# Kernel tuning notes

Measured on AMD Instinct MI355X. Metric: run time of the kernel, lower is better.

Reference implementation:

```python
import jax, jax.numpy as jnp
import numpy as np

B, L, D, H, DH = 2, 2048, 1024, 16, 64
THETA_T = 100.0
EPS_COS = 1e-6
EPS_NORM = 1e-6


def make_rope_tables(n_heads=H, d_head=DH, theta_t=THETA_T):
    dr = d_head // 12                      # 5 rotary freqs per head per axis
    n = n_heads * dr
    log_min, log_max = np.log(np.pi), np.log(10.0 * np.pi)
    f = np.exp(np.linspace(log_min, log_max, n + 1)[:-1])
    freqs = np.stack([f, f]).reshape(2, dr, n_heads).transpose(0, 2, 1)   # (2, H, dr)
    t_freqs = (theta_t ** (-np.arange(n, dtype=np.float64) / n)).reshape(dr, n_heads).T  # (H, dr)
    return jnp.asarray(freqs, jnp.float32), jnp.asarray(t_freqs, jnp.float32)


def rms_norm(x, scale, eps=EPS_NORM):
    ms = jnp.mean(x.astype(jnp.float32) ** 2, axis=-1, keepdims=True)
    return x * (scale.astype(jnp.float32) * jax.lax.rsqrt(ms + eps)).astype(x.dtype)


def rope_theta(pos, pos_orig, time, freqs, t_freqs):
    # pos_to_use: (b, l, c=2, xy=2), mapped to [-1, 1]
    pos_use = jnp.stack([pos_orig, pos], axis=2) * 2.0 - 1.0
    theta_w = pos_use[..., 0][:, :, :, None, None] * freqs[0]      # b l 2 H dr
    theta_h = pos_use[..., 1][:, :, :, None, None] * freqs[1]      # b l 2 H dr
    theta_t = time[:, :, None, None, None] * t_freqs               # b l 1 H dr
    theta = jnp.concatenate([theta_h, theta_w, theta_t], axis=2)   # b l 5 H dr
    b, l = theta.shape[0], theta.shape[1]
    theta = jnp.transpose(theta, (0, 1, 3, 2, 4)).reshape(b, l, H, -1)  # b l H (5*dr)
    return theta


def apply_rotary_emb(x, theta):
    d = theta.shape[-1]
    x1, x2, x3 = x[..., :d], x[..., d:2 * d], x[..., 2 * d:]
    cos, sin = jnp.cos(theta), jnp.sin(theta)
    y1 = x1 * cos - x2 * sin
    y2 = x2 * cos + x1 * sin
    return jnp.concatenate([y1, y2, x3], axis=-1)


def scale_for_cosine_sim(q, k, scale, eps=EPS_COS):
    sq = jnp.sum(q * q, axis=-1, keepdims=True)
    sk = jnp.sum(k * k, axis=-1, keepdims=True)
    sqrt_scale = jnp.sqrt(scale)                         # (H,1,1) -> broadcasts to (b,H,l,1)
    return q * (sqrt_scale * jax.lax.rsqrt(sq + eps)), k * (sqrt_scale * jax.lax.rsqrt(sk + eps))


def setup_inputs() -> dict:
    key = jax.random.key(0)
    ks = jax.random.split(key, 8)
    return {
        "x": jax.random.normal(ks[0], (B, L, D), jnp.float32),
        "pos": jax.random.uniform(ks[1], (B, L, 2), jnp.float32),
        "pos_orig": jax.random.uniform(ks[2], (B, L, 2), jnp.float32),
        "time": jax.random.uniform(ks[3], (B, L), jnp.float32),
        "w_qkv": jax.random.normal(ks[4], (3 * D, D), jnp.float32) * (D ** -0.5),
        "w_out": jax.random.normal(ks[5], (D, D), jnp.float32) * (D ** -0.5),
        "w_up": jax.random.normal(ks[6], (4 * D, D), jnp.float32) * (D ** -0.5),
        "w_down": jax.random.normal(ks[7], (D, 4 * D), jnp.float32) * ((4 * D) ** -0.5),
        "norm1_scale": jnp.ones((D,), jnp.float32),
        "norm2_scale": jnp.ones((D,), jnp.float32),
        "qk_scale": jnp.full((H, 1, 1), 10.0, jnp.float32),
    }


def reference(x, pos, pos_orig, time, w_qkv, w_out, w_up, w_down,
              norm1_scale, norm2_scale, qk_scale):
    freqs, t_freqs = make_rope_tables()
    b, l, _ = x.shape

    # --- attention block (pre-norm) ---
    xn = rms_norm(x, norm1_scale)
    qkv = jnp.einsum('bld,ed->ble', xn, w_qkv)                  # b l 3D
    q, k, v = jnp.split(qkv, 3, axis=-1)
    q = q.reshape(b, l, H, DH)
    k = k.reshape(b, l, H, DH)
    v = v.reshape(b, l, H, DH).transpose(0, 2, 1, 3)            # b H l dh

    theta = rope_theta(pos, pos_orig, time, freqs, t_freqs)      # b l H 25
    q = apply_rotary_emb(q, theta).transpose(0, 2, 1, 3)         # b H l dh
    k = apply_rotary_emb(k, theta).transpose(0, 2, 1, 3)

    q, k = scale_for_cosine_sim(q, k, qk_scale)                  # cosine-sim QK norm
    scores = jnp.einsum('bhqd,bhkd->bhqk', q, k)                 # scale=1 (already folded in)
    probs = jax.nn.softmax(scores, axis=-1)
    attn = jnp.einsum('bhqk,bhkd->bhqd', probs, v)
    attn = attn.transpose(0, 2, 1, 3).reshape(b, l, D)
    x = x + jnp.einsum('bld,ed->ble', attn, w_out)

    h = rms_norm(x, norm2_scale)
    h = jax.nn.gelu(jnp.einsum('bld,ed->ble', h, w_up), approximate=True)
    x = x + jnp.einsum('ble,de->bld', h, w_down)
    return x
```

## Files before the change

### kernel.cpp

```cpp
#include <hip/hip_runtime.h>

#define B_ 2
#define L_ 2048
#define D_ 1024
#define H_ 16
#define DH_ 64

typedef float f32x4 __attribute__((ext_vector_type(4)));
typedef __bf16 bf16x8 __attribute__((ext_vector_type(8)));

__device__ __forceinline__ ushort f2bf(float f) {
  unsigned u = __float_as_uint(f);
  u += 0x7fffu + ((u >> 16) & 1u);
  return (ushort)(u >> 16);
}
__device__ __forceinline__ float bf2f(ushort h) {
  return __uint_as_float(((unsigned)h) << 16);
}

__device__ __forceinline__ void gload_lds16(const void* g, void* l) {
  __builtin_amdgcn_global_load_lds(
      (const __attribute__((address_space(1))) unsigned*)g,
      (__attribute__((address_space(3))) unsigned*)l, 16, 0, 0);
}

__global__ __launch_bounds__(256) void cast_bf16_kernel(const float* __restrict__ in,
                                                        ushort* __restrict__ out, int n4) {
  int i = blockIdx.x * 256 + threadIdx.x;
  if (i >= n4) return;
  float4 v = ((const float4*)in)[i];
  ushort4 o;
  o.x = f2bf(v.x); o.y = f2bf(v.y); o.z = f2bf(v.z); o.w = f2bf(v.w);
  ((ushort4*)out)[i] = o;
}

__global__ __launch_bounds__(256) void rmsnorm_kernel(const float* __restrict__ x,
                                                      const float* __restrict__ scale,
                                                      ushort* __restrict__ out) {
  int row = blockIdx.x, t = threadIdx.x;
  float4 v = ((const float4*)(x + (size_t)row * D_))[t];
  float ss = v.x * v.x + v.y * v.y + v.z * v.z + v.w * v.w;
#pragma unroll
  for (int d = 1; d < 64; d <<= 1) ss += __shfl_xor(ss, d);
  __shared__ float wsum[4];
  if ((t & 63) == 0) wsum[t >> 6] = ss;
  __syncthreads();
  float tot = wsum[0] + wsum[1] + wsum[2] + wsum[3];
  float r = rsqrtf(tot * (1.0f / D_) + 1e-6f);
  float4 sc = ((const float4*)scale)[t];
  ushort4 o;
  o.x = f2bf(v.x * sc.x * r); o.y = f2bf(v.y * sc.y * r);
  o.z = f2bf(v.z * sc.z * r); o.w = f2bf(v.w * sc.w * r);
  ((ushort4*)(out + (size_t)row * D_))[t] = o;
}

template <int EPI, int BM, int BN, int DEPTH, int XR>
__global__ __launch_bounds__(256) void gemm_nt(const ushort* __restrict__ A,
                                               const ushort* __restrict__ Bw,
                                               void* __restrict__ Cout,
                                               const float* __restrict__ resid,
                                               int M, int N, int K) {
  constexpr int WROWS = BM / 2, WCOLS = BN / 2;
  constexpr int MR = WROWS / 16, NR = WCOLS / 16;
  constexpr int ALOADS = BM / 64, BLOADS = BN / 64;
  constexpr int NLOADS = ALOADS + BLOADS;
  constexpr int XC = 8 / XR;
  __shared__ __align__(16) ushort Als[DEPTH][BM * 32];
  __shared__ __align__(16) ushort Bls[DEPTH][BN * 32];
  const int tid = threadIdx.x;
  const int lane = tid & 63;
  const int w = tid >> 6;
  const int wr = w >> 1, wc = w & 1;
  const int bid = blockIdx.y * gridDim.x + blockIdx.x;
  const int xcd = bid & 7;
  const int i = bid >> 3;
  const int CR = gridDim.x / XR, CC = gridDim.y / XC;
  const int rt = (xcd % XR) * CR + (i % CR);
  const int ct = (xcd / XR) * CC + (i / CR);
  const int row0 = rt * BM;
  const int col0 = ct * BN;
  const ushort* Ab = A + (size_t)row0 * K;
  const ushort* Bb = Bw + (size_t)col0 * K;
  const int sr = tid >> 2;
  const int scA = (((tid & 3) ^ ((tid >> 3) & 3)) * 8);
  const int fr = lane & 15;
  const int fg = lane >> 4;
  f32x4 zero = {0.f, 0.f, 0.f, 0.f};
  f32x4 acc[MR][NR];
#pragma unroll
  for (int m = 0; m < MR; m++)
#pragma unroll
    for (int n = 0; n < NR; n++) acc[m][n] = zero;

  auto stage = [&](int buf, int kt) {
#pragma unroll
    for (int i2 = 0; i2 < ALOADS; i2++)
      gload_lds16(Ab + (size_t)(sr + 64 * i2) * K + kt + scA, &Als[buf][i2 * 2048 + tid * 8]);
#pragma unroll
    for (int i2 = 0; i2 < BLOADS; i2++)
      gload_lds16(Bb + (size_t)(sr + 64 * i2) * K + kt + scA, &Bls[buf][i2 * 2048 + tid * 8]);
  };
  const int nt = K >> 5;
#pragma unroll
  for (int p = 0; p < DEPTH - 1; p++) stage(p, p << 5);
  int cur = 0, sbuf = DEPTH - 1;
  for (int t = 0; t < nt; t++) {
    const int ahead = nt - 1 - t;
    if constexpr (DEPTH == 3) {
      if (ahead >= 1) asm volatile("s_waitcnt vmcnt(%0)" ::"i"(NLOADS) : "memory");
      else            asm volatile("s_waitcnt vmcnt(0)" ::: "memory");
    } else {
      if (ahead >= 3)      asm volatile("s_waitcnt vmcnt(%0)" ::"i"(3 * NLOADS) : "memory");
      else if (ahead == 2) asm volatile("s_waitcnt vmcnt(%0)" ::"i"(2 * NLOADS) : "memory");
      else if (ahead == 1) asm volatile("s_waitcnt vmcnt(%0)" ::"i"(NLOADS) : "memory");
      else                 asm volatile("s_waitcnt vmcnt(0)" ::: "memory");
    }
    __builtin_amdgcn_s_barrier();
    __builtin_amdgcn_sched_barrier(0);
    if (t + DEPTH - 1 < nt) {
      stage(sbuf, (t + DEPTH - 1) << 5);
      sbuf = (sbuf == DEPTH - 1) ? 0 : sbuf + 1;
    }
    bf16x8 af[MR], bfr[NR];
#pragma unroll
    for (int m = 0; m < MR; m++) {
      int rA = wr * WROWS + m * 16 + fr;
      af[m] = *(const bf16x8*)&Als[cur][rA * 32 + ((fg ^ ((rA >> 1) & 3)) << 3)];
    }
#pragma unroll
    for (int n = 0; n < NR; n++) {
      int rB = wc * WCOLS + n * 16 + fr;
      bfr[n] = *(const bf16x8*)&Bls[cur][rB * 32 + ((fg ^ ((rB >> 1) & 3)) << 3)];
    }
    __builtin_amdgcn_s_setprio(1);
#pragma unroll
    for (int m = 0; m < MR; m++)
#pragma unroll
      for (int n = 0; n < NR; n++)
        acc[m][n] = __builtin_amdgcn_mfma_f32_16x16x32_bf16(af[m], bfr[n], acc[m][n], 0, 0, 0);
    __builtin_amdgcn_s_setprio(0);
    cur = (cur == DEPTH - 1) ? 0 : cur + 1;
  }
  const int orow = row0 + wr * WROWS + fg * 4;
  const int ocol = col0 + wc * WCOLS + fr;
#pragma unroll
  for (int m = 0; m < MR; m++) {
#pragma unroll
    for (int j = 0; j < 4; j++) {
      int r = orow + m * 16 + j;
#pragma unroll
      for (int n = 0; n < NR; n++) {
        int cidx = ocol + n * 16;
        size_t idx = (size_t)r * N + cidx;
        float v = acc[m][n][j];
        if (EPI == 0) {
          ((ushort*)Cout)[idx] = f2bf(v);
        } else if (EPI == 1) {
          ((float*)Cout)[idx] = resid[idx] + v;
        } else {
          float g = 0.5f * v * (1.0f + tanhf(0.7978845608f * (v + 0.044715f * v * v * v)));
          ((ushort*)Cout)[idx] = f2bf(g);
        }
      }
    }
  }
}

__global__ __launch_bounds__(256) void rope_kernel(const ushort* __restrict__ qkv,
                                                   const float* __restrict__ pos,
                                                   const float* __restrict__ pos_orig,
                                                   const float* __restrict__ timep,
                                                   const float* __restrict__ qk_scale,
                                                   ushort* __restrict__ qr,
                                                   ushort* __restrict__ kr) {
  int gw = (blockIdx.x * 256 + threadIdx.x) >> 6;
  int lane = threadIdx.x & 63;
  int h = gw & 15;
  int row = gw >> 4;
  int b = row >> 11;
  int l = row & (L_ - 1);
  float qv = bf2f(qkv[(size_t)row * 3072 + h * 64 + lane]);
  float kv = bf2f(qkv[(size_t)row * 3072 + 1024 + h * 64 + lane]);
  float c = 1.0f, s = 0.0f;
  if (lane < 50) {
    int idx = lane < 25 ? lane : lane - 25;
    int sg = idx / 5, d = idx % 5;
    int fi = d * 16 + h;
    float th;
    if (sg == 4) {
      th = timep[row] * __expf(-(float)fi * 0.05756462732485115f);
    } else {
      float fr = 3.14159265358979323846f * __expf((float)fi * 0.028782313662425575f);
      const float* psrc = (sg == 0 || sg == 2) ? pos_orig : pos;
      int comp = (sg < 2) ? 1 : 0;
      th = (2.0f * psrc[(size_t)row * 2 + comp] - 1.0f) * fr;
    }
    s = sinf(th);
    c = cosf(th);
  }
  int partner = lane < 25 ? lane + 25 : lane - 25;
  float qp = __shfl(qv, partner, 64);
  float kp = __shfl(kv, partner, 64);
  float yq, yk;
  if (lane < 25) { yq = qv * c - qp * s; yk = kv * c - kp * s; }
  else if (lane < 50) { yq = qv * c + qp * s; yk = kv * c + kp * s; }
  else { yq = qv; yk = kv; }
  float sq = yq * yq, sk = yk * yk;
#pragma unroll
  for (int d = 1; d < 64; d <<= 1) { sq += __shfl_xor(sq, d); sk += __shfl_xor(sk, d); }
  float scl = sqrtf(qk_scale[h]);
  float qo = yq * scl * rsqrtf(sq + 1e-6f);
  float ko = yk * scl * rsqrtf(sk + 1e-6f);
  size_t o = ((size_t)(b * 16 + h) * L_ + l) * 64 + lane;
  qr[o] = f2bf(qo);
  kr[o] = f2bf(ko);
}

__global__ __launch_bounds__(256) void vtrans_kernel(const ushort* __restrict__ qkv,
                                                     ushort* __restrict__ vT) {
  __shared__ __align__(16) ushort tile[64][72];
  int t = threadIdx.x;
  int lt = blockIdx.x;
  int bh = blockIdx.y;
  int b = bh >> 4, h = bh & 15;
  int r = t >> 3, c0 = (t & 7) * 8;
#pragma unroll
  for (int half = 0; half < 2; half++) {
    const ushort* src =
        qkv + (size_t)(b * L_ + lt * 64 + r + half * 32) * 3072 + 2048 + h * 64 + c0;
    *(uint4*)&tile[r + half * 32][c0] = *(const uint4*)src;
  }
  __syncthreads();
#pragma unroll
  for (int half = 0; half < 2; half++) {
    int dh = r + half * 32;
    unsigned p0 = (unsigned)tile[c0 + 0][dh] | ((unsigned)tile[c0 + 1][dh] << 16);
    unsigned p1 = (unsigned)tile[c0 + 2][dh] | ((unsigned)tile[c0 + 3][dh] << 16);
    unsigned p2 = (unsigned)tile[c0 + 4][dh] | ((unsigned)tile[c0 + 5][dh] << 16);
    unsigned p3 = (unsigned)tile[c0 + 6][dh] | ((unsigned)tile[c0 + 7][dh] << 16);
    uint4 o; o.x = p0; o.y = p1; o.z = p2; o.w = p3;
    *(uint4*)&vT[((size_t)bh * 64 + dh) * L_ + lt * 64 + c0] = o;
  }
}

__global__ __launch_bounds__(256) void attn_kernel(const ushort* __restrict__ qr,
                                                   const ushort* __restrict__ kr,
                                                   const ushort* __restrict__ vT,
                                                   ushort* __restrict__ attnb) {
  __shared__ __align__(16) ushort Kls[2][64 * 64];
  __shared__ __align__(16) ushort Vls[2][64 * 64];
  __shared__ __align__(16) ushort Pls[4][16 * 64];
  const int tid = threadIdx.x, lane = tid & 63, w = tid >> 6;
  const int qt = blockIdx.x, bh = blockIdx.y;
  const int b = bh >> 4;
  const int fr = lane & 15, fg = lane >> 4;
  const ushort* Qb = qr + ((size_t)bh * L_ + qt * 64 + w * 16) * 64;
  bf16x8 qf[2];
#pragma unroll
  for (int c = 0; c < 2; c++)
    qf[c] = *(const bf16x8*)(Qb + fr * 64 + c * 32 + fg * 8);
  f32x4 zero = {0.f, 0.f, 0.f, 0.f};
  f32x4 accO[4];
#pragma unroll
  for (int n = 0; n < 4; n++) accO[n] = zero;
  float lrow[4] = {0.f, 0.f, 0.f, 0.f};
  const int sr = tid >> 3;
  const int scz = (((tid & 7) ^ (sr & 7)) * 8);
  auto stage = [&](int buf, int kt) {
    gload_lds16(kr + ((size_t)bh * L_ + kt + sr) * 64 + scz, &Kls[buf][tid * 8]);
    gload_lds16(kr + ((size_t)bh * L_ + kt + 32 + sr) * 64 + scz, &Kls[buf][2048 + tid * 8]);
    gload_lds16(vT + ((size_t)bh * 64 + sr) * L_ + kt + scz, &Vls[buf][tid * 8]);
    gload_lds16(vT + ((size_t)bh * 64 + 32 + sr) * L_ + kt + scz, &Vls[buf][2048 + tid * 8]);
  };
  stage(0, 0);
  int cur = 0;
  for (int t = 0; t < (L_ >> 6); t++) {
    asm volatile("s_waitcnt vmcnt(0)" ::: "memory");
    __builtin_amdgcn_s_barrier();
    __builtin_amdgcn_sched_barrier(0);
    if (t + 1 < (L_ >> 6)) stage(cur ^ 1, (t + 1) << 6);
    f32x4 sv[4];
#pragma unroll
    for (int n = 0; n < 4; n++) sv[n] = zero;
    __builtin_amdgcn_s_setprio(1);
#pragma unroll
    for (int c = 0; c < 2; c++) {
#pragma unroll
      for (int n = 0; n < 4; n++) {
        bf16x8 kf =
            *(const bf16x8*)&Kls[cur][(n * 16 + fr) * 64 + (((c * 4 + fg) ^ (fr & 7)) << 3)];
        sv[n] = __builtin_amdgcn_mfma_f32_16x16x32_bf16(qf[c], kf, sv[n], 0, 0, 0);
      }
    }
    __builtin_amdgcn_s_setprio(0);
#pragma unroll
    for (int n = 0; n < 4; n++)
#pragma unroll
      for (int j = 0; j < 4; j++) {
        float p = __expf(sv[n][j] - 12.0f);
        sv[n][j] = p;
        lrow[j] += p;
      }
#pragma unroll
    for (int j = 0; j < 4; j++) {
      int row = fg * 4 + j;
      int rbase = row * 64;
      int rx = row & 7;
#pragma unroll
      for (int n = 0; n < 4; n++) {
        int chunk = 2 * n + (fr >> 3);
        Pls[w][rbase + ((chunk ^ rx) << 3) + (fr & 7)] =
            (ushort)(__float_as_uint(sv[n][j]) >> 16);
      }
    }
    __builtin_amdgcn_s_setprio(1);
#pragma unroll
    for (int c = 0; c < 2; c++) {
      bf16x8 pa = *(const bf16x8*)&Pls[w][fr * 64 + (((c * 4 + fg) ^ (fr & 7)) << 3)];
#pragma unroll
      for (int n = 0; n < 4; n++) {
        bf16x8 vb =
            *(const bf16x8*)&Vls[cur][(n * 16 + fr) * 64 + (((c * 4 + fg) ^ (fr & 7)) << 3)];
        accO[n] = __builtin_amdgcn_mfma_f32_16x16x32_bf16(pa, vb, accO[n], 0, 0, 0);
      }
    }
    __builtin_amdgcn_s_setprio(0);
    cur ^= 1;
  }
#pragma unroll
  for (int j = 0; j < 4; j++) {
#pragma unroll
    for (int d = 1; d < 16; d <<= 1) lrow[j] += __shfl_xor(lrow[j], d);
    lrow[j] = 1.0f / lrow[j];
  }
#pragma unroll
  for (int n = 0; n < 4; n++) {
#pragma unroll
    for (int j = 0; j < 4; j++) {
      float o = accO[n][j] * lrow[j];
      int qrow = qt * 64 + w * 16 + fg * 4 + j;
      int dh = fr + n * 16;
      attnb[(size_t)(b * L_ + qrow) * 1024 + (bh & 15) * 64 + dh] = f2bf(o);
    }
  }
}

extern "C" void kernel_launch(void* const* d_in, const int* in_sizes, int n_in,
                              void* d_out, int out_size, void* d_ws, size_t ws_size,
                              hipStream_t stream) {
  const float* x = (const float*)d_in[0];
  const float* pos = (const float*)d_in[1];
  const float* pos_orig = (const float*)d_in[2];
  const float* timep = (const float*)d_in[3];
  const float* w_qkv = (const float*)d_in[4];
  const float* w_out = (const float*)d_in[5];
  const float* w_up = (const float*)d_in[6];
  const float* w_down = (const float*)d_in[7];
  const float* norm1 = (const float*)d_in[8];
  const float* norm2 = (const float*)d_in[9];
  const float* qk_scale = (const float*)d_in[10];
  float* out = (float*)d_out;
  char* ws = (char*)d_ws;
  size_t off = 0;
  auto alloc = [&](size_t bytes) {
    void* p = ws + off;
    off += bytes;
    return p;
  };
  ushort* xn = (ushort*)alloc(8ull << 20);
  ushort* qkvb = (ushort*)alloc(32ull << 20);
  ushort* qrb = (ushort*)alloc(8ull << 20);
  ushort* krb = (ushort*)alloc(8ull << 20);
  ushort* vTb = (ushort*)alloc(8ull << 20);
  ushort* attnb = (ushort*)alloc(8ull << 20);
  float* x1 = (float*)alloc(16ull << 20);
  ushort* wqkvb = (ushort*)alloc(6ull << 20);
  ushort* woutb = (ushort*)alloc(2ull << 20);
  ushort* wupb = (ushort*)alloc(8ull << 20);
  ushort* wdownb = (ushort*)alloc(8ull << 20);

  cast_bf16_kernel<<<3072, 256, 0, stream>>>(w_qkv, wqkvb, 3145728 / 4);
  cast_bf16_kernel<<<1024, 256, 0, stream>>>(w_out, woutb, 1048576 / 4);
  cast_bf16_kernel<<<4096, 256, 0, stream>>>(w_up, wupb, 4194304 / 4);
  cast_bf16_kernel<<<4096, 256, 0, stream>>>(w_down, wdownb, 4194304 / 4);

  rmsnorm_kernel<<<4096, 256, 0, stream>>>(x, norm1, xn);
  gemm_nt<0, 128, 128, 3, 4><<<dim3(32, 24), 256, 0, stream>>>(xn, wqkvb, qkvb, nullptr, 4096, 3072, 1024);
  rope_kernel<<<16384, 256, 0, stream>>>(qkvb, pos, pos_orig, timep, qk_scale, qrb, krb);
  vtrans_kernel<<<dim3(32, 32), 256, 0, stream>>>(qkvb, vTb);
  attn_kernel<<<dim3(32, 32), 256, 0, stream>>>(qrb, krb, vTb, attnb);
  gemm_nt<1, 64, 64, 5, 8><<<dim3(64, 16), 256, 0, stream>>>(attnb, woutb, x1, x, 4096, 1024, 1024);
  rmsnorm_kernel<<<4096, 256, 0, stream>>>(x1, norm2, xn);
  gemm_nt<2, 128, 128, 3, 4><<<dim3(32, 32), 256, 0, stream>>>(xn, wupb, qkvb, nullptr, 4096, 4096, 1024);
  gemm_nt<1, 64, 64, 5, 8><<<dim3(64, 16), 256, 0, stream>>>(qkvb, wdownb, out, x1, 4096, 1024, 4096);
}
```

Before: 299.4 us.

## Process two K-tiles per barrier in small GEMMs and remap attention blocks to XCDs

The GEMM main loop becomes a generalized pipeline in which each barrier iteration consumes SUB K-tiles and issues SUB prefetches. The 64x64 GEMMs (out-proj and down-proj) move from depth 5 with one tile per barrier to depth 6 with two tiles per barrier, halving the number of barriers and waitcnt points. The attention kernel also remaps its block index so that consecutive blocks on the same XCD share a batch-head, which should improve K/V reuse in that XCD's L2. In exchange, each wait covers fewer tiles in flight and the deeper ring uses more LDS.

```diff
diff --git a/kernel.cpp b/kernel.cpp
--- a/kernel.cpp
+++ b/kernel.cpp
@@ -54,7 +54,7 @@
   ((ushort4*)(out + (size_t)row * D_))[t] = o;
 }
 
-template <int EPI, int BM, int BN, int DEPTH, int XR>
+template <int EPI, int BM, int BN, int DEPTH, int SUB, int XR>
 __global__ __launch_bounds__(256) void gemm_nt(const ushort* __restrict__ A,
                                                const ushort* __restrict__ Bw,
                                                void* __restrict__ Cout,
@@ -64,6 +64,8 @@
   constexpr int MR = WROWS / 16, NR = WCOLS / 16;
   constexpr int ALOADS = BM / 64, BLOADS = BN / 64;
   constexpr int NLOADS = ALOADS + BLOADS;
+  constexpr int P = DEPTH - SUB;
+  constexpr int STEADY = NLOADS * (P - SUB);
   constexpr int XC = 8 / XR;
   __shared__ __align__(16) ushort Als[DEPTH][BM * 32];
   __shared__ __align__(16) ushort Bls[DEPTH][BN * 32];
@@ -73,10 +75,10 @@
   const int wr = w >> 1, wc = w & 1;
   const int bid = blockIdx.y * gridDim.x + blockIdx.x;
   const int xcd = bid & 7;
-  const int i = bid >> 3;
+  const int i0 = bid >> 3;
   const int CR = gridDim.x / XR, CC = gridDim.y / XC;
-  const int rt = (xcd % XR) * CR + (i % CR);
-  const int ct = (xcd / XR) * CC + (i / CR);
+  const int rt = (xcd % XR) * CR + (i0 % CR);
+  const int ct = (xcd / XR) * CC + (i0 / CR);
   const int row0 = rt * BM;
   const int col0 = ct * BN;
   const ushort* Ab = A + (size_t)row0 * K;
@@ -92,54 +94,50 @@
 #pragma unroll
     for (int n = 0; n < NR; n++) acc[m][n] = zero;
 
-  auto stage = [&](int buf, int kt) {
+  auto stage = [&](int slot, int kt) {
 #pragma unroll
     for (int i2 = 0; i2 < ALOADS; i2++)
-      gload_lds16(Ab + (size_t)(sr + 64 * i2) * K + kt + scA, &Als[buf][i2 * 2048 + tid * 8]);
+      gload_lds16(Ab + (size_t)(sr + 64 * i2) * K + kt + scA, &Als[slot][i2 * 2048 + tid * 8]);
 #pragma unroll
     for (int i2 = 0; i2 < BLOADS; i2++)
-      gload_lds16(Bb + (size_t)(sr + 64 * i2) * K + kt + scA, &Bls[buf][i2 * 2048 + tid * 8]);
+      gload_lds16(Bb + (size_t)(sr + 64 * i2) * K + kt + scA, &Bls[slot][i2 * 2048 + tid * 8]);
   };
   const int nt = K >> 5;
-#pragma unroll
-  for (int p = 0; p < DEPTH - 1; p++) stage(p, p << 5);
-  int cur = 0, sbuf = DEPTH - 1;
-  for (int t = 0; t < nt; t++) {
-    const int ahead = nt - 1 - t;
-    if constexpr (DEPTH == 3) {
-      if (ahead >= 1) asm volatile("s_waitcnt vmcnt(%0)" ::"i"(NLOADS) : "memory");
-      else            asm volatile("s_waitcnt vmcnt(0)" ::: "memory");
-    } else {
-      if (ahead >= 3)      asm volatile("s_waitcnt vmcnt(%0)" ::"i"(3 * NLOADS) : "memory");
-      else if (ahead == 2) asm volatile("s_waitcnt vmcnt(%0)" ::"i"(2 * NLOADS) : "memory");
-      else if (ahead == 1) asm volatile("s_waitcnt vmcnt(%0)" ::"i"(NLOADS) : "memory");
-      else                 asm volatile("s_waitcnt vmcnt(0)" ::: "memory");
-    }
+  const int ni = nt / SUB;
+#pragma unroll
+  for (int p = 0; p < P; p++) stage(p, p << 5);
+  for (int t = 0; t < ni; t++) {
+    if (t < ni - 1) asm volatile("s_waitcnt vmcnt(%0)" ::"i"(STEADY) : "memory");
+    else            asm volatile("s_waitcnt vmcnt(0)" ::: "memory");
     __builtin_amdgcn_s_barrier();
     __builtin_amdgcn_sched_barrier(0);
-    if (t + DEPTH - 1 < nt) {
-      stage(sbuf, (t + DEPTH - 1) << 5);
-      sbuf = (sbuf == DEPTH - 1) ? 0 : sbuf + 1;
-    }
-    bf16x8 af[MR], bfr[NR];
-#pragma unroll
-    for (int m = 0; m < MR; m++) {
-      int rA = wr * WROWS + m * 16 + fr;
-      af[m] = *(const bf16x8*)&Als[cur][rA * 32 + ((fg ^ ((rA >> 1) & 3)) << 3)];
-    }
-#pragma unroll
-    for (int n = 0; n < NR; n++) {
-      int rB = wc * WCOLS + n * 16 + fr;
-      bfr[n] = *(const bf16x8*)&Bls[cur][rB * 32 + ((fg ^ ((rB >> 1) & 3)) << 3)];
-    }
-    __builtin_amdgcn_s_setprio(1);
-#pragma unroll
-    for (int m = 0; m < MR; m++)
-#pragma unroll
-      for (int n = 0; n < NR; n++)
-        acc[m][n] = __builtin_amdgcn_mfma_f32_16x16x32_bf16(af[m], bfr[n], acc[m][n], 0, 0, 0);
-    __builtin_amdgcn_s_setprio(0);
-    cur = (cur == DEPTH - 1) ? 0 : cur + 1;
+#pragma unroll
+    for (int j = 0; j < SUB; j++) {
+      int s = SUB * t + P + j;
+      if (s < nt) stage(s % DEPTH, s << 5);
+    }
+#pragma unroll
+    for (int j = 0; j < SUB; j++) {
+      const int cur = (SUB * t + j) % DEPTH;
+      bf16x8 af[MR], bfr[NR];
+#pragma unroll
+      for (int m = 0; m < MR; m++) {
+        int rA = wr * WROWS + m * 16 + fr;
+        af[m] = *(const bf16x8*)&Als[cur][rA * 32 + ((fg ^ ((rA >> 1) & 3)) << 3)];
+      }
+#pragma unroll
+      for (int n = 0; n < NR; n++) {
+        int rB = wc * WCOLS + n * 16 + fr;
+        bfr[n] = *(const bf16x8*)&Bls[cur][rB * 32 + ((fg ^ ((rB >> 1) & 3)) << 3)];
+      }
+      __builtin_amdgcn_s_setprio(1);
+#pragma unroll
+      for (int m = 0; m < MR; m++)
+#pragma unroll
+        for (int n = 0; n < NR; n++)
+          acc[m][n] = __builtin_amdgcn_mfma_f32_16x16x32_bf16(af[m], bfr[n], acc[m][n], 0, 0, 0);
+      __builtin_amdgcn_s_setprio(0);
+    }
   }
   const int orow = row0 + wr * WROWS + fg * 4;
   const int ocol = col0 + wc * WCOLS + fr;
@@ -251,7 +249,9 @@
   __shared__ __align__(16) ushort Vls[2][64 * 64];
   __shared__ __align__(16) ushort Pls[4][16 * 64];
   const int tid = threadIdx.x, lane = tid & 63, w = tid >> 6;
-  const int qt = blockIdx.x, bh = blockIdx.y;
+  const int bid = blockIdx.y * gridDim.x + blockIdx.x;
+  const int qt = (bid >> 3) & 31;
+  const int bh = (bid & 7) | ((bid >> 8) << 3);
   const int b = bh >> 4;
   const int fr = lane & 15, fg = lane >> 4;
   const ushort* Qb = qr + ((size_t)bh * L_ + qt * 64 + w * 16) * 64;
@@ -385,12 +385,12 @@
   cast_bf16_kernel<<<4096, 256, 0, stream>>>(w_down, wdownb, 4194304 / 4);
 
   rmsnorm_kernel<<<4096, 256, 0, stream>>>(x, norm1, xn);
-  gemm_nt<0, 128, 128, 3, 4><<<dim3(32, 24), 256, 0, stream>>>(xn, wqkvb, qkvb, nullptr, 4096, 3072, 1024);
+  gemm_nt<0, 128, 128, 3, 1, 4><<<dim3(32, 24), 256, 0, stream>>>(xn, wqkvb, qkvb, nullptr, 4096, 3072, 1024);
   rope_kernel<<<16384, 256, 0, stream>>>(qkvb, pos, pos_orig, timep, qk_scale, qrb, krb);
   vtrans_kernel<<<dim3(32, 32), 256, 0, stream>>>(qkvb, vTb);
   attn_kernel<<<dim3(32, 32), 256, 0, stream>>>(qrb, krb, vTb, attnb);
-  gemm_nt<1, 64, 64, 5, 8><<<dim3(64, 16), 256, 0, stream>>>(attnb, woutb, x1, x, 4096, 1024, 1024);
+  gemm_nt<1, 64, 64, 6, 2, 8><<<dim3(64, 16), 256, 0, stream>>>(attnb, woutb, x1, x, 4096, 1024, 1024);
   rmsnorm_kernel<<<4096, 256, 0, stream>>>(x1, norm2, xn);
-  gemm_nt<2, 128, 128, 3, 4><<<dim3(32, 32), 256, 0, stream>>>(xn, wupb, qkvb, nullptr, 4096, 4096, 1024);
-  gemm_nt<1, 64, 64, 5, 8><<<dim3(64, 16), 256, 0, stream>>>(qkvb, wdownb, out, x1, 4096, 1024, 4096);
-}
+  gemm_nt<2, 128, 128, 3, 1, 4><<<dim3(32, 32), 256, 0, stream>>>(xn, wupb, qkvb, nullptr, 4096, 4096, 1024);
+  gemm_nt<1, 64, 64, 6, 2, 8><<<dim3(64, 16), 256, 0, stream>>>(qkvb, wdownb, out, x1, 4096, 1024, 4096);
+}
```

Result: slower. 322.3 us (+7.6%).
